# Kernel tuning notes

Hardware: AMD Instinct MI355X
Metric: run time of the kernel (lower is better)

The kernel has to match this reference:

```python
import jax, jax.numpy as jnp
import numpy as np

B, N, D, DH = 8, 2048, 1024, 64

def setup_inputs() -> dict:
    key = jax.random.key(0)
    ks = jax.random.split(key, 4)
    s = 1.0 / np.sqrt(D)
    return {
        "x": jax.random.normal(ks[0], (B, N, D), dtype=jnp.float32),
        "Wq": jax.random.normal(ks[1], (D, DH), dtype=jnp.float32) * s,
        "bq": jnp.zeros((DH,), dtype=jnp.float32),
        "Wk": jax.random.normal(ks[2], (D, DH), dtype=jnp.float32) * s,
        "bk": jnp.zeros((DH,), dtype=jnp.float32),
        "Wv": jax.random.normal(ks[3], (D, DH), dtype=jnp.float32) * s,
        "bv": jnp.zeros((DH,), dtype=jnp.float32),
    }

def reference(x, Wq, bq, Wk, bk, Wv, bv):
    # Projections: [B,N,DH]
    Q = x @ Wq + bq
    K = x @ Wk + bk
    V = x @ Wv + bv
    sqrt_dh = jnp.sqrt(jnp.asarray(DH, dtype=x.dtype))
    # scores[b,i,j] = Q_i . K_j  (original materializes [B,N,N,DH]; GEMM is equivalent math)
    att = jnp.einsum("bid,bjd->bij", Q, K) / sqrt_dh
    # NOTE: original softmaxes over dim=1 (the query/i axis), not the usual j axis.
    att = jax.nn.softmax(att, axis=1)
    # Dropout is identity in eval mode.
    return jnp.einsum("bij,bjd->bid", att, V)
```

## Files before the change

kernel.cpp:

```cpp
#include <hip/hip_runtime.h>
#include <math.h>

#define Bn  8
#define Nn  2048
#define Dn  1024
#define DHn 64
#define PAD  72
#define PADP 72

typedef __attribute__((ext_vector_type(8))) short bf16x8;
typedef __attribute__((ext_vector_type(4))) float f32x4;

static __device__ inline short f2bf(float f) {
    unsigned u = __builtin_bit_cast(unsigned, f);
    u += 0x7FFFu + ((u >> 16) & 1u);
    return (short)(u >> 16);
}
static __device__ inline bf16x8 pack8(float4 a, float4 b) {
    bf16x8 v;
    v[0] = f2bf(a.x); v[1] = f2bf(a.y); v[2] = f2bf(a.z); v[3] = f2bf(a.w);
    v[4] = f2bf(b.x); v[5] = f2bf(b.y); v[6] = f2bf(b.z); v[7] = f2bf(b.w);
    return v;
}

__global__ __launch_bounds__(128) void wt_kernel(
    const float* __restrict__ Wq, const float* __restrict__ Wk,
    const float* __restrict__ Wv, short* __restrict__ Wtf)
{
    const int nt = blockIdx.x / 16, kt = blockIdx.x % 16;
    const int t = threadIdx.x;
    const int half = t >> 6, l = t & 63;
    const int c = l & 15, quad = l >> 4;
    const int mat = nt >> 2, cm = (nt & 3) * 16 + c;
    const float* Wm = (mat == 0) ? Wq : (mat == 1 ? Wk : Wv);
    short* o = &Wtf[((((size_t)nt * 16 + kt) * 2 + half) * 64 + l) * 8];
#pragma unroll
    for (int e = 0; e < 8; ++e) {
        const int k = kt * 64 + half * 32 + quad * 8 + e;
        o[e] = f2bf(Wm[(size_t)k * DHn + cm]);
    }
}

__global__ __launch_bounds__(256) void qkv_kernel(
    const float* __restrict__ x, const short* __restrict__ Wtf,
    const float* __restrict__ bq, const float* __restrict__ bk,
    const float* __restrict__ bv,
    short* __restrict__ Qb, short* __restrict__ Kb, float* __restrict__ Vtf32)
{
    __shared__ __attribute__((aligned(16))) short xs[2][32][PAD];

    const int t = threadIdx.x;
    const int w = t >> 6, l = t & 63;
    const int c = l & 15, quad = l >> 4;
    const int ibase = blockIdx.x * 32;
    const int r0 = t >> 3, kc = t & 7;

    const float* xrow = &x[(size_t)(ibase + r0) * Dn + kc * 8];

    {
        const float4 a = ((const float4*)xrow)[0];
        const float4 b = ((const float4*)xrow)[1];
        *(bf16x8*)&xs[0][r0][kc * 8] = pack8(a, b);
    }

    f32x4 acc[2][3];
#pragma unroll
    for (int mt = 0; mt < 2; ++mt)
#pragma unroll
        for (int nt = 0; nt < 3; ++nt) acc[mt][nt] = (f32x4){0.f, 0.f, 0.f, 0.f};

    __syncthreads();

    for (int kt = 0; kt < 16; ++kt) {
        const int cur = kt & 1;
        float4 pa, pb;
        if (kt < 15) {
            pa = ((const float4*)(xrow + (kt + 1) * 64))[0];
            pb = ((const float4*)(xrow + (kt + 1) * 64))[1];
        }
#pragma unroll
        for (int h = 0; h < 2; ++h) {
            const bf16x8 af0 = *(const bf16x8*)&xs[cur][c][h * 32 + quad * 8];
            const bf16x8 af1 = *(const bf16x8*)&xs[cur][16 + c][h * 32 + quad * 8];
#pragma unroll
            for (int nt = 0; nt < 3; ++nt) {
                const int ntg = w * 3 + nt;
                const bf16x8 bf = *(const bf16x8*)&Wtf[((((size_t)ntg * 16 + kt) * 2 + h) * 64 + l) * 8];
                acc[0][nt] = __builtin_amdgcn_mfma_f32_16x16x32_bf16(af0, bf, acc[0][nt], 0, 0, 0);
                acc[1][nt] = __builtin_amdgcn_mfma_f32_16x16x32_bf16(af1, bf, acc[1][nt], 0, 0, 0);
            }
        }
        if (kt < 15) *(bf16x8*)&xs[1 - cur][r0][kc * 8] = pack8(pa, pb);
        __syncthreads();
    }

#pragma unroll
    for (int nt = 0; nt < 3; ++nt) {
        const int col = w * 48 + nt * 16 + c;
        const int mat = col >> 6, cm = col & 63;
        const float bias = (mat == 0 ? bq : (mat == 1 ? bk : bv))[cm];
#pragma unroll
        for (int mt = 0; mt < 2; ++mt) {
            if (mat == 2) {
                const int row = ibase + mt * 16 + quad * 4;
                const int b = row >> 11, i = row & (Nn - 1);
                float4 o;
                o.x = acc[mt][nt][0] + bias;
                o.y = acc[mt][nt][1] + bias;
                o.z = acc[mt][nt][2] + bias;
                o.w = acc[mt][nt][3] + bias;
                *(float4*)&Vtf32[((size_t)b * DHn + cm) * Nn + i] = o;
            } else {
                const float s = (mat == 1) ? 0.125f : 1.0f;
                short* Out = (mat == 0) ? Qb : Kb;
#pragma unroll
                for (int r = 0; r < 4; ++r)
                    Out[(size_t)(ibase + mt * 16 + quad * 4 + r) * DHn + cm] =
                        f2bf((acc[mt][nt][r] + bias) * s);
            }
        }
    }
}

__global__ __launch_bounds__(256) void colsum_kernel(
    const short* __restrict__ Qb, const short* __restrict__ Kb,
    float* __restrict__ lpart)
{
    __shared__ __attribute__((aligned(16))) short Qw[4][2][32][PAD];
    __shared__ float red[16][64];

    const int t = threadIdx.x;
    const int w = t >> 6, l = t & 63;
    const int c = l & 15, quad = l >> 4;
    const int bid = blockIdx.x;
    const int b = bid & 7, jt = (bid >> 3) & 31, s = (bid >> 8) & 3;
    const int jbase = jt * 64;
    const int srow = l >> 1, scoff = (l & 1) * 32;

    bf16x8 kb[4][2];
#pragma unroll
    for (int nt = 0; nt < 4; ++nt)
#pragma unroll
        for (int kk = 0; kk < 2; ++kk)
            kb[nt][kk] = *(const bf16x8*)&Kb[((size_t)b * Nn + jbase + nt * 16 + c) * DHn
                                             + kk * 32 + quad * 8];

    const short* qbase = &Qb[((size_t)b * Nn + s * 512 + w * 128 + srow) * DHn + scoff];

#pragma unroll
    for (int k = 0; k < 4; ++k)
        *(bf16x8*)&Qw[w][0][srow][scoff + k * 8] = *(const bf16x8*)(qbase + k * 8);

    float lsum[4] = {0.f, 0.f, 0.f, 0.f};

    for (int it2 = 0; it2 < 4; ++it2) {
        const int cur = it2 & 1;
        bf16x8 p[4];
        if (it2 < 3) {
            const short* pq = qbase + (size_t)(it2 + 1) * 32 * DHn;
#pragma unroll
            for (int k = 0; k < 4; ++k) p[k] = *(const bf16x8*)(pq + k * 8);
        }
#pragma unroll
        for (int cc2 = 0; cc2 < 2; ++cc2) {
            const bf16x8 aq0 = *(const bf16x8*)&Qw[w][cur][cc2 * 16 + c][quad * 8];
            const bf16x8 aq1 = *(const bf16x8*)&Qw[w][cur][cc2 * 16 + c][32 + quad * 8];
#pragma unroll
            for (int nt = 0; nt < 4; ++nt) {
                f32x4 sv = (f32x4){0.f, 0.f, 0.f, 0.f};
                sv = __builtin_amdgcn_mfma_f32_16x16x32_bf16(aq0, kb[nt][0], sv, 0, 0, 0);
                sv = __builtin_amdgcn_mfma_f32_16x16x32_bf16(aq1, kb[nt][1], sv, 0, 0, 0);
                lsum[nt] += __expf(sv[0]) + __expf(sv[1]) + __expf(sv[2]) + __expf(sv[3]);
            }
        }
        if (it2 < 3) {
#pragma unroll
            for (int k = 0; k < 4; ++k)
                *(bf16x8*)&Qw[w][1 - cur][srow][scoff + k * 8] = p[k];
        }
    }

#pragma unroll
    for (int nt = 0; nt < 4; ++nt) red[w * 4 + quad][nt * 16 + c] = lsum[nt];
    __syncthreads();
    if (t < 64) {
        float sum = 0.f;
#pragma unroll
        for (int r = 0; r < 16; ++r) sum += red[r][t];
        lpart[((size_t)s * Bn + b) * Nn + jbase + t] = sum;
    }
}

__global__ __launch_bounds__(256) void vscale_kernel(
    const float* __restrict__ lpart, const float* __restrict__ Vtf32,
    short* __restrict__ Vt)
{
    const int idx = blockIdx.x * 256 + threadIdx.x;
    const int b = idx >> 14;
    const int d = (idx >> 8) & 63;
    const int j0 = (idx & 255) * 8;
    const size_t off = ((size_t)b * DHn + d) * Nn + j0;
    const size_t lj = (size_t)b * Nn + j0;

    const float* l0 = &lpart[lj];
    float4 sa = ((const float4*)l0)[0];
    float4 sb = ((const float4*)l0)[1];
#pragma unroll
    for (int s = 1; s < 4; ++s) {
        const float4 a = ((const float4*)(l0 + (size_t)s * Bn * Nn))[0];
        const float4 c = ((const float4*)(l0 + (size_t)s * Bn * Nn))[1];
        sa.x += a.x; sa.y += a.y; sa.z += a.z; sa.w += a.w;
        sb.x += c.x; sb.y += c.y; sb.z += c.z; sb.w += c.w;
    }
    float4 va = ((const float4*)&Vtf32[off])[0];
    float4 vb = ((const float4*)&Vtf32[off])[1];
    va.x /= sa.x; va.y /= sa.y; va.z /= sa.z; va.w /= sa.w;
    vb.x /= sb.x; vb.y /= sb.y; vb.z /= sb.z; vb.w /= sb.w;
    *(bf16x8*)&Vt[off] = pack8(va, vb);
}

__global__ __launch_bounds__(256) void attnout_kernel(
    const short* __restrict__ Qb, const short* __restrict__ Kb,
    const short* __restrict__ Vt, float* __restrict__ outp)
{
    __shared__ __attribute__((aligned(16))) short Ks[2][64][PAD];
    __shared__ __attribute__((aligned(16))) short Vs[2][64][PAD];
    __shared__ __attribute__((aligned(16))) short Pt[4][2][16][PADP];

    const int t = threadIdx.x;
    const int w = t >> 6, lane = t & 63;
    const int c = lane & 15, quad = lane >> 4;
    const int bid = blockIdx.x;
    const int b = bid & 7, rem = bid >> 3, it = rem >> 2, s = rem & 3;
    const int ibase = it * 128;
    const int r0 = t >> 2, cc = (t & 3) * 16;

    bf16x8 aq[2][2];
#pragma unroll
    for (int sub = 0; sub < 2; ++sub) {
        const size_t qrow = (size_t)b * Nn + ibase + w * 32 + sub * 16 + c;
        aq[sub][0] = *(const bf16x8*)&Qb[qrow * DHn + quad * 8];
        aq[sub][1] = *(const bf16x8*)&Qb[qrow * DHn + 32 + quad * 8];
    }

    const short* kbase = &Kb[((size_t)b * Nn + s * 512 + r0) * DHn + cc];
    const short* vbase = &Vt[((size_t)b * DHn + r0) * Nn + s * 512 + cc];

    *(bf16x8*)&Ks[0][r0][cc]     = *(const bf16x8*)kbase;
    *(bf16x8*)&Ks[0][r0][cc + 8] = *(const bf16x8*)(kbase + 8);
    *(bf16x8*)&Vs[0][r0][cc]     = *(const bf16x8*)vbase;
    *(bf16x8*)&Vs[0][r0][cc + 8] = *(const bf16x8*)(vbase + 8);

    f32x4 acc[2][4];
#pragma unroll
    for (int sub = 0; sub < 2; ++sub)
#pragma unroll
        for (int dn = 0; dn < 4; ++dn) acc[sub][dn] = (f32x4){0.f, 0.f, 0.f, 0.f};
    __syncthreads();

    for (int jt2 = 0; jt2 < 8; ++jt2) {
        const int cur = jt2 & 1;
        bf16x8 pk0, pk1, pv0, pv1;
        if (jt2 < 7) {
            const short* pk = kbase + (size_t)(jt2 + 1) * 64 * DHn;
            pk0 = *(const bf16x8*)pk; pk1 = *(const bf16x8*)(pk + 8);
            const short* pv = vbase + (jt2 + 1) * 64;
            pv0 = *(const bf16x8*)pv; pv1 = *(const bf16x8*)(pv + 8);
        }

#pragma unroll
        for (int nt = 0; nt < 4; ++nt) {
            const bf16x8 kb0 = *(const bf16x8*)&Ks[cur][nt * 16 + c][quad * 8];
            const bf16x8 kb1 = *(const bf16x8*)&Ks[cur][nt * 16 + c][32 + quad * 8];
#pragma unroll
            for (int sub = 0; sub < 2; ++sub) {
                f32x4 sv = (f32x4){0.f, 0.f, 0.f, 0.f};
                sv = __builtin_amdgcn_mfma_f32_16x16x32_bf16(kb0, aq[sub][0], sv, 0, 0, 0);
                sv = __builtin_amdgcn_mfma_f32_16x16x32_bf16(kb1, aq[sub][1], sv, 0, 0, 0);
                ushort4 o;
                o.x = (unsigned short)f2bf(__expf(sv[0]));
                o.y = (unsigned short)f2bf(__expf(sv[1]));
                o.z = (unsigned short)f2bf(__expf(sv[2]));
                o.w = (unsigned short)f2bf(__expf(sv[3]));
                *(ushort4*)&Pt[w][sub][c][nt * 16 + quad * 4] = o;
            }
        }
        bf16x8 ap[2][2];
#pragma unroll
        for (int sub = 0; sub < 2; ++sub) {
            ap[sub][0] = *(const bf16x8*)&Pt[w][sub][c][quad * 8];
            ap[sub][1] = *(const bf16x8*)&Pt[w][sub][c][32 + quad * 8];
        }
#pragma unroll
        for (int dn = 0; dn < 4; ++dn) {
            const bf16x8 vb0 = *(const bf16x8*)&Vs[cur][dn * 16 + c][quad * 8];
            const bf16x8 vb1 = *(const bf16x8*)&Vs[cur][dn * 16 + c][32 + quad * 8];
#pragma unroll
            for (int sub = 0; sub < 2; ++sub) {
                acc[sub][dn] = __builtin_amdgcn_mfma_f32_16x16x32_bf16(ap[sub][0], vb0, acc[sub][dn], 0, 0, 0);
                acc[sub][dn] = __builtin_amdgcn_mfma_f32_16x16x32_bf16(ap[sub][1], vb1, acc[sub][dn], 0, 0, 0);
            }
        }

        if (jt2 < 7) {
            *(bf16x8*)&Ks[1 - cur][r0][cc]     = pk0;
            *(bf16x8*)&Ks[1 - cur][r0][cc + 8] = pk1;
            *(bf16x8*)&Vs[1 - cur][r0][cc]     = pv0;
            *(bf16x8*)&Vs[1 - cur][r0][cc + 8] = pv1;
        }
        __syncthreads();
    }

    float* op = outp + (size_t)s * (Bn * Nn * DHn) + ((size_t)b * Nn + ibase) * DHn;
#pragma unroll
    for (int sub = 0; sub < 2; ++sub)
#pragma unroll
        for (int dn = 0; dn < 4; ++dn)
#pragma unroll
            for (int r = 0; r < 4; ++r)
                op[(w * 32 + sub * 16 + quad * 4 + r) * DHn + dn * 16 + c] = acc[sub][dn][r];
}

__global__ __launch_bounds__(256) void outreduce_kernel(
    const float* __restrict__ outp, float* __restrict__ out)
{
    const int id = blockIdx.x * 256 + threadIdx.x;
    const float4* p = (const float4*)outp;
    float4 r = p[id];
#pragma unroll
    for (int k = 1; k < 4; ++k) {
        const float4 a = p[id + (size_t)k * 262144];
        r.x += a.x; r.y += a.y; r.z += a.z; r.w += a.w;
    }
    ((float4*)out)[id] = r;
}

extern "C" void kernel_launch(void* const* d_in, const int* in_sizes, int n_in,
                              void* d_out, int out_size, void* d_ws, size_t ws_size,
                              hipStream_t stream)
{
    const float* x  = (const float*)d_in[0];
    const float* Wq = (const float*)d_in[1];
    const float* bq = (const float*)d_in[2];
    const float* Wk = (const float*)d_in[3];
    const float* bk = (const float*)d_in[4];
    const float* Wv = (const float*)d_in[5];
    const float* bv = (const float*)d_in[6];
    float* out = (float*)d_out;

    char* ws = (char*)d_ws;
    short* Qb    = (short*)(ws);
    short* Kb    = (short*)(ws + (size_t)(1 << 21));
    short* Vt    = (short*)(ws + (size_t)(2 << 21));
    short* Wtf   = (short*)(ws + (size_t)(3 << 21));
    float* lpart = (float*)(ws + (size_t)(3 << 21) + (1 << 19));
    float* Vtf32 = (float*)(ws + (size_t)(7 << 20));
    float* outp  = (float*)(ws + (size_t)(11 << 20));

    wt_kernel<<<dim3(192), dim3(128), 0, stream>>>(Wq, Wk, Wv, Wtf);
    qkv_kernel<<<dim3(512), dim3(256), 0, stream>>>(x, Wtf, bq, bk, bv, Qb, Kb, Vtf32);
    colsum_kernel<<<dim3(1024), dim3(256), 0, stream>>>(Qb, Kb, lpart);
    vscale_kernel<<<dim3(512), dim3(256), 0, stream>>>(lpart, Vtf32, Vt);
    attnout_kernel<<<dim3(512), dim3(256), 0, stream>>>(Qb, Kb, Vt, outp);
    outreduce_kernel<<<dim3(1024), dim3(256), 0, stream>>>(outp, out);
}
```

Baseline: 151.7 us.

## Fuse split reductions into producer kernels via last-block atomic counters

Removes the separate vscale and outreduce kernels. The last of the four split blocks for each tile, detected with an atomic counter plus threadfence, now does the column-sum normalisation of V and the output partial-sum reduction itself. Counters are zeroed inside the weight-transpose kernel. The weight transpose is staged through shared memory for coalesced loads and vector stores, and the QKV GEMM prefetches x four k-steps ahead in registers. This saves two launches and their tail latency, at the cost of serialized tail work in the last-arriving blocks and more register pressure.

```diff
diff --git a/kernel.cpp b/kernel.cpp
--- a/kernel.cpp
+++ b/kernel.cpp
@@ -25,20 +25,31 @@
 
 __global__ __launch_bounds__(128) void wt_kernel(
     const float* __restrict__ Wq, const float* __restrict__ Wk,
-    const float* __restrict__ Wv, short* __restrict__ Wtf)
-{
+    const float* __restrict__ Wv, short* __restrict__ Wtf, int* __restrict__ cnt)
+{
+    __shared__ float wsm[64][20];
     const int nt = blockIdx.x / 16, kt = blockIdx.x % 16;
     const int t = threadIdx.x;
+    const int gid = blockIdx.x * 128 + t;
+    if (gid < 384) cnt[gid] = 0;
+
+    const int mat = nt >> 2;
+    const float* Wm = (mat == 0) ? Wq : (mat == 1 ? Wk : Wv);
+    {
+        const int k = t >> 1, n8 = (t & 1) * 8;
+        const float* src = &Wm[(size_t)(kt * 64 + k) * DHn + (nt & 3) * 16 + n8];
+        const float4 f0 = ((const float4*)src)[0];
+        const float4 f1 = ((const float4*)src)[1];
+        *(float4*)&wsm[k][n8]     = f0;
+        *(float4*)&wsm[k][n8 + 4] = f1;
+    }
+    __syncthreads();
     const int half = t >> 6, l = t & 63;
     const int c = l & 15, quad = l >> 4;
-    const int mat = nt >> 2, cm = (nt & 3) * 16 + c;
-    const float* Wm = (mat == 0) ? Wq : (mat == 1 ? Wk : Wv);
-    short* o = &Wtf[((((size_t)nt * 16 + kt) * 2 + half) * 64 + l) * 8];
-#pragma unroll
-    for (int e = 0; e < 8; ++e) {
-        const int k = kt * 64 + half * 32 + quad * 8 + e;
-        o[e] = f2bf(Wm[(size_t)k * DHn + cm]);
-    }
+    bf16x8 o;
+#pragma unroll
+    for (int e = 0; e < 8; ++e) o[e] = f2bf(wsm[half * 32 + quad * 8 + e][c]);
+    *(bf16x8*)&Wtf[((((size_t)nt * 16 + kt) * 2 + half) * 64 + l) * 8] = o;
 }
 
 __global__ __launch_bounds__(256) void qkv_kernel(
@@ -63,6 +74,13 @@
         *(bf16x8*)&xs[0][r0][kc * 8] = pack8(a, b);
     }
 
+    float4 ra[4], rb[4];
+#pragma unroll
+    for (int k = 1; k <= 3; ++k) {
+        ra[k] = ((const float4*)(xrow + k * 64))[0];
+        rb[k] = ((const float4*)(xrow + k * 64))[1];
+    }
+
     f32x4 acc[2][3];
 #pragma unroll
     for (int mt = 0; mt < 2; ++mt)
@@ -71,12 +89,12 @@
 
     __syncthreads();
 
+#pragma unroll
     for (int kt = 0; kt < 16; ++kt) {
         const int cur = kt & 1;
-        float4 pa, pb;
-        if (kt < 15) {
-            pa = ((const float4*)(xrow + (kt + 1) * 64))[0];
-            pb = ((const float4*)(xrow + (kt + 1) * 64))[1];
+        if (kt + 4 <= 15) {
+            ra[kt & 3] = ((const float4*)(xrow + (kt + 4) * 64))[0];
+            rb[kt & 3] = ((const float4*)(xrow + (kt + 4) * 64))[1];
         }
 #pragma unroll
         for (int h = 0; h < 2; ++h) {
@@ -90,7 +108,8 @@
                 acc[1][nt] = __builtin_amdgcn_mfma_f32_16x16x32_bf16(af1, bf, acc[1][nt], 0, 0, 0);
             }
         }
-        if (kt < 15) *(bf16x8*)&xs[1 - cur][r0][kc * 8] = pack8(pa, pb);
+        if (kt < 15)
+            *(bf16x8*)&xs[1 - cur][r0][kc * 8] = pack8(ra[(kt + 1) & 3], rb[(kt + 1) & 3]);
         __syncthreads();
     }
 
@@ -124,7 +143,8 @@
 
 __global__ __launch_bounds__(256) void colsum_kernel(
     const short* __restrict__ Qb, const short* __restrict__ Kb,
-    float* __restrict__ lpart)
+    const float* __restrict__ Vtf32, float* __restrict__ lpart,
+    short* __restrict__ Vt, int* __restrict__ cnt)
 {
     __shared__ __attribute__((aligned(16))) short Qw[4][2][32][PAD];
     __shared__ float red[16][64];
@@ -189,43 +209,44 @@
         for (int r = 0; r < 16; ++r) sum += red[r][t];
         lpart[((size_t)s * Bn + b) * Nn + jbase + t] = sum;
     }
-}
-
-__global__ __launch_bounds__(256) void vscale_kernel(
-    const float* __restrict__ lpart, const float* __restrict__ Vtf32,
-    short* __restrict__ Vt)
-{
-    const int idx = blockIdx.x * 256 + threadIdx.x;
-    const int b = idx >> 14;
-    const int d = (idx >> 8) & 63;
-    const int j0 = (idx & 255) * 8;
-    const size_t off = ((size_t)b * DHn + d) * Nn + j0;
-    const size_t lj = (size_t)b * Nn + j0;
-
-    const float* l0 = &lpart[lj];
-    float4 sa = ((const float4*)l0)[0];
-    float4 sb = ((const float4*)l0)[1];
-#pragma unroll
-    for (int s = 1; s < 4; ++s) {
-        const float4 a = ((const float4*)(l0 + (size_t)s * Bn * Nn))[0];
-        const float4 c = ((const float4*)(l0 + (size_t)s * Bn * Nn))[1];
-        sa.x += a.x; sa.y += a.y; sa.z += a.z; sa.w += a.w;
-        sb.x += c.x; sb.y += c.y; sb.z += c.z; sb.w += c.w;
-    }
-    float4 va = ((const float4*)&Vtf32[off])[0];
-    float4 vb = ((const float4*)&Vtf32[off])[1];
-    va.x /= sa.x; va.y /= sa.y; va.z /= sa.z; va.w /= sa.w;
-    vb.x /= sb.x; vb.y /= sb.y; vb.z /= sb.z; vb.w /= sb.w;
-    *(bf16x8*)&Vt[off] = pack8(va, vb);
+
+    __threadfence();
+    __syncthreads();
+    if (t == 0) {
+        const int old = atomicAdd(&cnt[b * 32 + jt], 1);
+        red[0][0] = (old == 3) ? 1.0f : 0.0f;
+    }
+    __syncthreads();
+    if (red[0][0] != 0.0f) {
+        __threadfence();
+        const int d = t >> 2, jc = (t & 3) * 16;
+        const float* lp = &lpart[(size_t)b * Nn + jbase + jc];
+        float lsum16[16];
+#pragma unroll
+        for (int jj = 0; jj < 16; ++jj)
+            lsum16[jj] = lp[jj] + lp[(size_t)Bn * Nn + jj]
+                       + lp[2 * (size_t)Bn * Nn + jj] + lp[3 * (size_t)Bn * Nn + jj];
+        const size_t voff = ((size_t)b * DHn + d) * Nn + jbase + jc;
+        const float4* vsrc = (const float4*)&Vtf32[voff];
+        float4 a0 = vsrc[0], a1 = vsrc[1], a2 = vsrc[2], a3 = vsrc[3];
+        a0.x /= lsum16[0];  a0.y /= lsum16[1];  a0.z /= lsum16[2];  a0.w /= lsum16[3];
+        a1.x /= lsum16[4];  a1.y /= lsum16[5];  a1.z /= lsum16[6];  a1.w /= lsum16[7];
+        a2.x /= lsum16[8];  a2.y /= lsum16[9];  a2.z /= lsum16[10]; a2.w /= lsum16[11];
+        a3.x /= lsum16[12]; a3.y /= lsum16[13]; a3.z /= lsum16[14]; a3.w /= lsum16[15];
+        *(bf16x8*)&Vt[voff]     = pack8(a0, a1);
+        *(bf16x8*)&Vt[voff + 8] = pack8(a2, a3);
+    }
 }
 
 __global__ __launch_bounds__(256) void attnout_kernel(
     const short* __restrict__ Qb, const short* __restrict__ Kb,
-    const short* __restrict__ Vt, float* __restrict__ outp)
+    const short* __restrict__ Vt, float* __restrict__ outp,
+    float* __restrict__ out, int* __restrict__ cnt)
 {
     __shared__ __attribute__((aligned(16))) short Ks[2][64][PAD];
     __shared__ __attribute__((aligned(16))) short Vs[2][64][PAD];
     __shared__ __attribute__((aligned(16))) short Pt[4][2][16][PADP];
+    __shared__ int lastf;
 
     const int t = threadIdx.x;
     const int w = t >> 6, lane = t & 63;
@@ -319,20 +340,29 @@
 #pragma unroll
             for (int r = 0; r < 4; ++r)
                 op[(w * 32 + sub * 16 + quad * 4 + r) * DHn + dn * 16 + c] = acc[sub][dn][r];
-}
-
-__global__ __launch_bounds__(256) void outreduce_kernel(
-    const float* __restrict__ outp, float* __restrict__ out)
-{
-    const int id = blockIdx.x * 256 + threadIdx.x;
-    const float4* p = (const float4*)outp;
-    float4 r = p[id];
-#pragma unroll
-    for (int k = 1; k < 4; ++k) {
-        const float4 a = p[id + (size_t)k * 262144];
-        r.x += a.x; r.y += a.y; r.z += a.z; r.w += a.w;
-    }
-    ((float4*)out)[id] = r;
+
+    __threadfence();
+    __syncthreads();
+    if (t == 0) lastf = (atomicAdd(&cnt[b * 16 + it], 1) == 3);
+    __syncthreads();
+    if (lastf) {
+        __threadfence();
+        const size_t base = (((size_t)b * Nn + ibase) * DHn) >> 2;
+        const float4* P = (const float4*)outp;
+        float4* O = (float4*)out;
+        const size_t sstride = ((size_t)Bn * Nn * DHn) >> 2;
+#pragma unroll
+        for (int k = 0; k < 8; ++k) {
+            const size_t idx = base + k * 256 + t;
+            float4 r = P[idx];
+#pragma unroll
+            for (int s2 = 1; s2 < 4; ++s2) {
+                const float4 a2 = P[idx + (size_t)s2 * sstride];
+                r.x += a2.x; r.y += a2.y; r.z += a2.z; r.w += a2.w;
+            }
+            O[idx] = r;
+        }
+    }
 }
 
 extern "C" void kernel_launch(void* const* d_in, const int* in_sizes, int n_in,
@@ -354,13 +384,12 @@
     short* Vt    = (short*)(ws + (size_t)(2 << 21));
     short* Wtf   = (short*)(ws + (size_t)(3 << 21));
     float* lpart = (float*)(ws + (size_t)(3 << 21) + (1 << 19));
+    int*   cnt   = (int*)  (ws + (size_t)(3 << 21) + (1 << 19) + (1 << 18));
     float* Vtf32 = (float*)(ws + (size_t)(7 << 20));
     float* outp  = (float*)(ws + (size_t)(11 << 20));
 
-    wt_kernel<<<dim3(192), dim3(128), 0, stream>>>(Wq, Wk, Wv, Wtf);
+    wt_kernel<<<dim3(192), dim3(128), 0, stream>>>(Wq, Wk, Wv, Wtf, cnt);
     qkv_kernel<<<dim3(512), dim3(256), 0, stream>>>(x, Wtf, bq, bk, bv, Qb, Kb, Vtf32);
-    colsum_kernel<<<dim3(1024), dim3(256), 0, stream>>>(Qb, Kb, lpart);
-    vscale_kernel<<<dim3(512), dim3(256), 0, stream>>>(lpart, Vtf32, Vt);
-    attnout_kernel<<<dim3(512), dim3(256), 0, stream>>>(Qb, Kb, Vt, outp);
-    outreduce_kernel<<<dim3(1024), dim3(256), 0, stream>>>(outp, out);
-}
+    colsum_kernel<<<dim3(1024), dim3(256), 0, stream>>>(Qb, Kb, Vtf32, lpart, Vt, cnt);
+    attnout_kernel<<<dim3(512), dim3(256), 0, stream>>>(Qb, Kb, Vt, outp, out, cnt + 256);
+}
```

Result: slower. 294.7 us (+94.2%).

## Drop LDS staging for K/V/Q, deepen x prefetch, coalesce weight transpose

Applied to the files above, without the earlier changes.

The attention-output kernel now has each wave own 16 query rows instead of 32 and reads K and V fragments straight from global/L2 rather than staging them through double-buffered LDS. This removes block-wide barriers, and the grid doubles to keep occupancy up. The colsum kernel likewise reads Q fragments directly from global memory. The QKV projection prefetches x four tiles ahead in registers, and the weight-transpose kernel stages through LDS so its global reads coalesce. The trade-off is more redundant global/L2 traffic for K/V, since there is less reuse per block, and higher register pressure.

```diff
diff --git a/kernel.cpp b/kernel.cpp
--- a/kernel.cpp
+++ b/kernel.cpp
@@ -27,18 +27,27 @@
     const float* __restrict__ Wq, const float* __restrict__ Wk,
     const float* __restrict__ Wv, short* __restrict__ Wtf)
 {
+    __shared__ float wsm[64][20];
     const int nt = blockIdx.x / 16, kt = blockIdx.x % 16;
     const int t = threadIdx.x;
+
+    const int mat = nt >> 2;
+    const float* Wm = (mat == 0) ? Wq : (mat == 1 ? Wk : Wv);
+    {
+        const int k = t >> 1, n8 = (t & 1) * 8;
+        const float* src = &Wm[(size_t)(kt * 64 + k) * DHn + (nt & 3) * 16 + n8];
+        const float4 f0 = ((const float4*)src)[0];
+        const float4 f1 = ((const float4*)src)[1];
+        *(float4*)&wsm[k][n8]     = f0;
+        *(float4*)&wsm[k][n8 + 4] = f1;
+    }
+    __syncthreads();
     const int half = t >> 6, l = t & 63;
     const int c = l & 15, quad = l >> 4;
-    const int mat = nt >> 2, cm = (nt & 3) * 16 + c;
-    const float* Wm = (mat == 0) ? Wq : (mat == 1 ? Wk : Wv);
-    short* o = &Wtf[((((size_t)nt * 16 + kt) * 2 + half) * 64 + l) * 8];
-#pragma unroll
-    for (int e = 0; e < 8; ++e) {
-        const int k = kt * 64 + half * 32 + quad * 8 + e;
-        o[e] = f2bf(Wm[(size_t)k * DHn + cm]);
-    }
+    bf16x8 o;
+#pragma unroll
+    for (int e = 0; e < 8; ++e) o[e] = f2bf(wsm[half * 32 + quad * 8 + e][c]);
+    *(bf16x8*)&Wtf[((((size_t)nt * 16 + kt) * 2 + half) * 64 + l) * 8] = o;
 }
 
 __global__ __launch_bounds__(256) void qkv_kernel(
@@ -63,6 +72,13 @@
         *(bf16x8*)&xs[0][r0][kc * 8] = pack8(a, b);
     }
 
+    float4 ra[4], rb[4];
+#pragma unroll
+    for (int k = 1; k <= 3; ++k) {
+        ra[k] = ((const float4*)(xrow + k * 64))[0];
+        rb[k] = ((const float4*)(xrow + k * 64))[1];
+    }
+
     f32x4 acc[2][3];
 #pragma unroll
     for (int mt = 0; mt < 2; ++mt)
@@ -71,12 +87,12 @@
 
     __syncthreads();
 
+#pragma unroll
     for (int kt = 0; kt < 16; ++kt) {
         const int cur = kt & 1;
-        float4 pa, pb;
-        if (kt < 15) {
-            pa = ((const float4*)(xrow + (kt + 1) * 64))[0];
-            pb = ((const float4*)(xrow + (kt + 1) * 64))[1];
+        if (kt + 4 <= 15) {
+            ra[kt & 3] = ((const float4*)(xrow + (kt + 4) * 64))[0];
+            rb[kt & 3] = ((const float4*)(xrow + (kt + 4) * 64))[1];
         }
 #pragma unroll
         for (int h = 0; h < 2; ++h) {
@@ -90,7 +106,8 @@
                 acc[1][nt] = __builtin_amdgcn_mfma_f32_16x16x32_bf16(af1, bf, acc[1][nt], 0, 0, 0);
             }
         }
-        if (kt < 15) *(bf16x8*)&xs[1 - cur][r0][kc * 8] = pack8(pa, pb);
+        if (kt < 15)
+            *(bf16x8*)&xs[1 - cur][r0][kc * 8] = pack8(ra[(kt + 1) & 3], rb[(kt + 1) & 3]);
         __syncthreads();
     }
 
@@ -126,16 +143,14 @@
     const short* __restrict__ Qb, const short* __restrict__ Kb,
     float* __restrict__ lpart)
 {
-    __shared__ __attribute__((aligned(16))) short Qw[4][2][32][PAD];
     __shared__ float red[16][64];
 
     const int t = threadIdx.x;
     const int w = t >> 6, l = t & 63;
     const int c = l & 15, quad = l >> 4;
     const int bid = blockIdx.x;
-    const int b = bid & 7, jt = (bid >> 3) & 31, s = (bid >> 8) & 3;
+    const int b = bid & 7, jt = (bid >> 3) & 31, s = bid >> 8;
     const int jbase = jt * 64;
-    const int srow = l >> 1, scoff = (l & 1) * 32;
 
     bf16x8 kb[4][2];
 #pragma unroll
@@ -145,26 +160,17 @@
             kb[nt][kk] = *(const bf16x8*)&Kb[((size_t)b * Nn + jbase + nt * 16 + c) * DHn
                                              + kk * 32 + quad * 8];
 
-    const short* qbase = &Qb[((size_t)b * Nn + s * 512 + w * 128 + srow) * DHn + scoff];
-
-#pragma unroll
-    for (int k = 0; k < 4; ++k)
-        *(bf16x8*)&Qw[w][0][srow][scoff + k * 8] = *(const bf16x8*)(qbase + k * 8);
+    const short* qb0 = &Qb[((size_t)b * Nn + s * 512 + w * 128 + c) * DHn];
 
     float lsum[4] = {0.f, 0.f, 0.f, 0.f};
 
+#pragma unroll
     for (int it2 = 0; it2 < 4; ++it2) {
-        const int cur = it2 & 1;
-        bf16x8 p[4];
-        if (it2 < 3) {
-            const short* pq = qbase + (size_t)(it2 + 1) * 32 * DHn;
-#pragma unroll
-            for (int k = 0; k < 4; ++k) p[k] = *(const bf16x8*)(pq + k * 8);
-        }
 #pragma unroll
         for (int cc2 = 0; cc2 < 2; ++cc2) {
-            const bf16x8 aq0 = *(const bf16x8*)&Qw[w][cur][cc2 * 16 + c][quad * 8];
-            const bf16x8 aq1 = *(const bf16x8*)&Qw[w][cur][cc2 * 16 + c][32 + quad * 8];
+            const short* qr = qb0 + (size_t)(it2 * 32 + cc2 * 16) * DHn;
+            const bf16x8 aq0 = *(const bf16x8*)(qr + quad * 8);
+            const bf16x8 aq1 = *(const bf16x8*)(qr + 32 + quad * 8);
 #pragma unroll
             for (int nt = 0; nt < 4; ++nt) {
                 f32x4 sv = (f32x4){0.f, 0.f, 0.f, 0.f};
@@ -173,11 +179,6 @@
                 lsum[nt] += __expf(sv[0]) + __expf(sv[1]) + __expf(sv[2]) + __expf(sv[3]);
             }
         }
-        if (it2 < 3) {
-#pragma unroll
-            for (int k = 0; k < 4; ++k)
-                *(bf16x8*)&Qw[w][1 - cur][srow][scoff + k * 8] = p[k];
-        }
     }
 
 #pragma unroll
@@ -223,102 +224,62 @@
     const short* __restrict__ Qb, const short* __restrict__ Kb,
     const short* __restrict__ Vt, float* __restrict__ outp)
 {
-    __shared__ __attribute__((aligned(16))) short Ks[2][64][PAD];
-    __shared__ __attribute__((aligned(16))) short Vs[2][64][PAD];
     __shared__ __attribute__((aligned(16))) short Pt[4][2][16][PADP];
 
     const int t = threadIdx.x;
     const int w = t >> 6, lane = t & 63;
     const int c = lane & 15, quad = lane >> 4;
     const int bid = blockIdx.x;
-    const int b = bid & 7, rem = bid >> 3, it = rem >> 2, s = rem & 3;
-    const int ibase = it * 128;
-    const int r0 = t >> 2, cc = (t & 3) * 16;
-
-    bf16x8 aq[2][2];
-#pragma unroll
-    for (int sub = 0; sub < 2; ++sub) {
-        const size_t qrow = (size_t)b * Nn + ibase + w * 32 + sub * 16 + c;
-        aq[sub][0] = *(const bf16x8*)&Qb[qrow * DHn + quad * 8];
-        aq[sub][1] = *(const bf16x8*)&Qb[qrow * DHn + 32 + quad * 8];
-    }
-
-    const short* kbase = &Kb[((size_t)b * Nn + s * 512 + r0) * DHn + cc];
-    const short* vbase = &Vt[((size_t)b * DHn + r0) * Nn + s * 512 + cc];
-
-    *(bf16x8*)&Ks[0][r0][cc]     = *(const bf16x8*)kbase;
-    *(bf16x8*)&Ks[0][r0][cc + 8] = *(const bf16x8*)(kbase + 8);
-    *(bf16x8*)&Vs[0][r0][cc]     = *(const bf16x8*)vbase;
-    *(bf16x8*)&Vs[0][r0][cc + 8] = *(const bf16x8*)(vbase + 8);
-
-    f32x4 acc[2][4];
-#pragma unroll
-    for (int sub = 0; sub < 2; ++sub)
-#pragma unroll
-        for (int dn = 0; dn < 4; ++dn) acc[sub][dn] = (f32x4){0.f, 0.f, 0.f, 0.f};
-    __syncthreads();
-
+    const int b = bid & 7, it = (bid >> 3) & 31, s = bid >> 8;
+    const int ibase = it * 64;
+
+    const size_t qrow = (size_t)b * Nn + ibase + w * 16 + c;
+    const bf16x8 aq0 = *(const bf16x8*)&Qb[qrow * DHn + quad * 8];
+    const bf16x8 aq1 = *(const bf16x8*)&Qb[qrow * DHn + 32 + quad * 8];
+
+    const short* K0 = &Kb[((size_t)b * Nn + s * 512) * DHn];
+    const short* V0 = &Vt[(size_t)b * DHn * Nn + s * 512];
+
+    f32x4 acc[4];
+#pragma unroll
+    for (int dn = 0; dn < 4; ++dn) acc[dn] = (f32x4){0.f, 0.f, 0.f, 0.f};
+
+#pragma unroll 2
     for (int jt2 = 0; jt2 < 8; ++jt2) {
         const int cur = jt2 & 1;
-        bf16x8 pk0, pk1, pv0, pv1;
-        if (jt2 < 7) {
-            const short* pk = kbase + (size_t)(jt2 + 1) * 64 * DHn;
-            pk0 = *(const bf16x8*)pk; pk1 = *(const bf16x8*)(pk + 8);
-            const short* pv = vbase + (jt2 + 1) * 64;
-            pv0 = *(const bf16x8*)pv; pv1 = *(const bf16x8*)(pv + 8);
-        }
-
 #pragma unroll
         for (int nt = 0; nt < 4; ++nt) {
-            const bf16x8 kb0 = *(const bf16x8*)&Ks[cur][nt * 16 + c][quad * 8];
-            const bf16x8 kb1 = *(const bf16x8*)&Ks[cur][nt * 16 + c][32 + quad * 8];
-#pragma unroll
-            for (int sub = 0; sub < 2; ++sub) {
-                f32x4 sv = (f32x4){0.f, 0.f, 0.f, 0.f};
-                sv = __builtin_amdgcn_mfma_f32_16x16x32_bf16(kb0, aq[sub][0], sv, 0, 0, 0);
-                sv = __builtin_amdgcn_mfma_f32_16x16x32_bf16(kb1, aq[sub][1], sv, 0, 0, 0);
-                ushort4 o;
-                o.x = (unsigned short)f2bf(__expf(sv[0]));
-                o.y = (unsigned short)f2bf(__expf(sv[1]));
-                o.z = (unsigned short)f2bf(__expf(sv[2]));
-                o.w = (unsigned short)f2bf(__expf(sv[3]));
-                *(ushort4*)&Pt[w][sub][c][nt * 16 + quad * 4] = o;
-            }
-        }
-        bf16x8 ap[2][2];
-#pragma unroll
-        for (int sub = 0; sub < 2; ++sub) {
-            ap[sub][0] = *(const bf16x8*)&Pt[w][sub][c][quad * 8];
-            ap[sub][1] = *(const bf16x8*)&Pt[w][sub][c][32 + quad * 8];
-        }
+            const short* kr = K0 + (size_t)(jt2 * 64 + nt * 16 + c) * DHn;
+            const bf16x8 kb0 = *(const bf16x8*)(kr + quad * 8);
+            const bf16x8 kb1 = *(const bf16x8*)(kr + 32 + quad * 8);
+            f32x4 sv = (f32x4){0.f, 0.f, 0.f, 0.f};
+            sv = __builtin_amdgcn_mfma_f32_16x16x32_bf16(kb0, aq0, sv, 0, 0, 0);
+            sv = __builtin_amdgcn_mfma_f32_16x16x32_bf16(kb1, aq1, sv, 0, 0, 0);
+            ushort4 o;
+            o.x = (unsigned short)f2bf(__expf(sv[0]));
+            o.y = (unsigned short)f2bf(__expf(sv[1]));
+            o.z = (unsigned short)f2bf(__expf(sv[2]));
+            o.w = (unsigned short)f2bf(__expf(sv[3]));
+            *(ushort4*)&Pt[w][cur][c][nt * 16 + quad * 4] = o;
+        }
+        const bf16x8 ap0 = *(const bf16x8*)&Pt[w][cur][c][quad * 8];
+        const bf16x8 ap1 = *(const bf16x8*)&Pt[w][cur][c][32 + quad * 8];
 #pragma unroll
         for (int dn = 0; dn < 4; ++dn) {
-            const bf16x8 vb0 = *(const bf16x8*)&Vs[cur][dn * 16 + c][quad * 8];
-            const bf16x8 vb1 = *(const bf16x8*)&Vs[cur][dn * 16 + c][32 + quad * 8];
-#pragma unroll
-            for (int sub = 0; sub < 2; ++sub) {
-                acc[sub][dn] = __builtin_amdgcn_mfma_f32_16x16x32_bf16(ap[sub][0], vb0, acc[sub][dn], 0, 0, 0);
-                acc[sub][dn] = __builtin_amdgcn_mfma_f32_16x16x32_bf16(ap[sub][1], vb1, acc[sub][dn], 0, 0, 0);
-            }
-        }
-
-        if (jt2 < 7) {
-            *(bf16x8*)&Ks[1 - cur][r0][cc]     = pk0;
-            *(bf16x8*)&Ks[1 - cur][r0][cc + 8] = pk1;
-            *(bf16x8*)&Vs[1 - cur][r0][cc]     = pv0;
-            *(bf16x8*)&Vs[1 - cur][r0][cc + 8] = pv1;
-        }
-        __syncthreads();
+            const short* vr = V0 + (size_t)(dn * 16 + c) * Nn + jt2 * 64;
+            const bf16x8 vb0 = *(const bf16x8*)(vr + quad * 8);
+            const bf16x8 vb1 = *(const bf16x8*)(vr + 32 + quad * 8);
+            acc[dn] = __builtin_amdgcn_mfma_f32_16x16x32_bf16(ap0, vb0, acc[dn], 0, 0, 0);
+            acc[dn] = __builtin_amdgcn_mfma_f32_16x16x32_bf16(ap1, vb1, acc[dn], 0, 0, 0);
+        }
     }
 
     float* op = outp + (size_t)s * (Bn * Nn * DHn) + ((size_t)b * Nn + ibase) * DHn;
 #pragma unroll
-    for (int sub = 0; sub < 2; ++sub)
-#pragma unroll
-        for (int dn = 0; dn < 4; ++dn)
-#pragma unroll
-            for (int r = 0; r < 4; ++r)
-                op[(w * 32 + sub * 16 + quad * 4 + r) * DHn + dn * 16 + c] = acc[sub][dn][r];
+    for (int dn = 0; dn < 4; ++dn)
+#pragma unroll
+        for (int r = 0; r < 4; ++r)
+            op[(w * 16 + quad * 4 + r) * DHn + dn * 16 + c] = acc[dn][r];
 }
 
 __global__ __launch_bounds__(256) void outreduce_kernel(
@@ -361,6 +322,6 @@
     qkv_kernel<<<dim3(512), dim3(256), 0, stream>>>(x, Wtf, bq, bk, bv, Qb, Kb, Vtf32);
     colsum_kernel<<<dim3(1024), dim3(256), 0, stream>>>(Qb, Kb, lpart);
     vscale_kernel<<<dim3(512), dim3(256), 0, stream>>>(lpart, Vtf32, Vt);
-    attnout_kernel<<<dim3(512), dim3(256), 0, stream>>>(Qb, Kb, Vt, outp);
+    attnout_kernel<<<dim3(1024), dim3(256), 0, stream>>>(Qb, Kb, Vt, outp);
     outreduce_kernel<<<dim3(1024), dim3(256), 0, stream>>>(outp, out);
 }
```

Result: slower. 197.7 us (+30.3%).
